# Performance work log

Hardware: AMD Instinct MI355X
Metric: run time of the kernel (lower is better)

Reference implementation:

```python
import jax, jax.numpy as jnp
import numpy as np

GRID = 16
N = GRID * GRID          # num_nodes = 256
D = 64                   # embed_dim
SPARSITY = 0.8
BATCH = 2048


def setup_inputs() -> dict:
    key = jax.random.key(0)
    ks = jax.random.split(key, 11)
    s1 = 1.0 / np.sqrt(D)          # fan_in of per-node Linears
    s2 = 1.0 / np.sqrt(N * D)      # fan_in of global_pool first Linear
    x = jax.random.normal(ks[0], (BATCH, N * D), dtype=jnp.float32)
    adj_param = jax.random.normal(ks[1], (N, N), dtype=jnp.float32) * 0.1
    W1 = jax.random.uniform(ks[2], (N, D, D), minval=-s1, maxval=s1, dtype=jnp.float32)
    b1 = jax.random.uniform(ks[3], (N, D), minval=-s1, maxval=s1, dtype=jnp.float32)
    W2 = jax.random.uniform(ks[4], (N, D, D), minval=-s1, maxval=s1, dtype=jnp.float32)
    b2 = jax.random.uniform(ks[5], (N, D), minval=-s1, maxval=s1, dtype=jnp.float32)
    gpW1 = jax.random.uniform(ks[6], (N * D, D), minval=-s2, maxval=s2, dtype=jnp.float32)
    gpb1 = jax.random.uniform(ks[7], (D,), minval=-s2, maxval=s2, dtype=jnp.float32)
    gpW2 = jax.random.uniform(ks[8], (D, D // 2), minval=-s1, maxval=s1, dtype=jnp.float32)
    gpb2 = jax.random.uniform(ks[9], (D // 2,), minval=-s1, maxval=s1, dtype=jnp.float32)
    return {"x": x, "adj_param": adj_param, "W1": W1, "b1": b1, "W2": W2, "b2": b2,
            "gpW1": gpW1, "gpb1": gpb1, "gpW2": gpW2, "gpb2": gpb2}


def _adjacency(adj_param):
    adj = jax.nn.sigmoid(adj_param)
    # threshold = sorted(flat adj)[int(sparsity * N*N)], then hard-threshold, then zero diagonal
    thr = jnp.sort(adj.reshape(-1))[int(SPARSITY * N * N)]
    adj = adj * (adj > thr)
    return adj * (1.0 - jnp.eye(N, dtype=adj.dtype))


def reference(x, adj_param, W1, b1, W2, b2, gpW1, gpb1, gpW2, gpb2):
    B = x.shape[0]
    adj = _adjacency(adj_param)
    xn = x.reshape(B, N, D)                                    # [B, N, D]
    # per-node distinct MLP == grouped GEMM with weights [N, D, D]
    h = jax.nn.relu(jnp.einsum('bnd,nde->bne', xn, W1) + b1)   # [B, N, D]
    node = jnp.einsum('bnd,nde->bne', h, W2) + b2              # [B, N, D]
    # adjacency-weighted neighbor sum: mixed[b,i] = sum_j adj[i,j] * node[b,j]
    mixed = jnp.einsum('ij,bjd->bid', adj, node)               # [B, N, D]
    final = 0.5 * mixed + 0.5 * node                           # residual mix
    g = jax.nn.relu(final.reshape(B, N * D) @ gpW1 + gpb1)     # [B, D]
    out = g @ gpW2 + gpb2                                      # [B, D//2]
    return out, adj
```

## Files before the change

### kernel.cpp

```cpp
#include <hip/hip_runtime.h>
#include <math.h>

typedef unsigned int uint;
typedef unsigned short ushort;
typedef short short8 __attribute__((ext_vector_type(8)));
typedef float f32x4 __attribute__((ext_vector_type(4)));

#define B_ 2048
#define N_ 256
#define D_ 64
#define ND_ 16384
#define NN_ 65536
#define KIDX_ 52428u
#define NGROUPS 32

#define WS_W1T    ((size_t)0)
#define WS_W2T    ((size_t)2*1024*1024)
#define WS_EFF    ((size_t)4*1024*1024)
#define WS_GPARTS ((size_t)8*1024*1024)
#define WS_SCAL   ((size_t)24*1024*1024)

__device__ __forceinline__ ushort f2bf(float f) {
    uint u = __float_as_uint(f);
    u += 0x7fffu + ((u >> 16) & 1u);
    return (ushort)(u >> 16);
}
__device__ __forceinline__ float bf2f(ushort u) { return __uint_as_float(((uint)u) << 16); }

__device__ __forceinline__ float sigmoid_exact(float a) {
    float t = (float)exp(-(double)a);
    return 1.0f / (1.0f + t);
}

__device__ __forceinline__ uint f2key(uint bits) {
    return bits ^ ((bits & 0x80000000u) ? 0xFFFFFFFFu : 0x80000000u);
}

__device__ __forceinline__ int wfrag_off(int e, int k) {
    return ((((e >> 4) * 2 + (k >> 5)) * 4 + ((k >> 3) & 3)) * 16 + (e & 15)) * 8 + (k & 7);
}

__device__ __forceinline__ int afrag_off(int jl, int i) {
    return (((((jl >> 4) * 8 + (i >> 5)) * 4 + ((i >> 3) & 3)) * 16) + (jl & 15)) * 8 + (i & 7);
}

__global__ __launch_bounds__(1024) void k_cvt_radix(const float* __restrict__ W1,
                                                    const float* __restrict__ W2,
                                                    const float* __restrict__ adj_param,
                                                    ushort* __restrict__ W1f,
                                                    ushort* __restrict__ W2f,
                                                    uint* __restrict__ scal) {
    __shared__ uint SH[16402] __attribute__((aligned(16)));
    int bid = blockIdx.x, tid = threadIdx.x;

    if (bid != 0) {
        int q = tid >> 8, t = tid & 255;
        int m = (bid - 1) * 4 + q;
        ushort* P = (ushort*)SH + q * 4096;
        const float* src = (m < 256) ? W1 + (size_t)m * 4096 : W2 + (size_t)(m - 256) * 4096;
#pragma unroll
        for (int i = 0; i < 16; i++) {
            int idx = i * 256 + t;
            int k = idx >> 6, e = idx & 63;
            P[wfrag_off(e, k)] = f2bf(src[idx]);
        }
        __syncthreads();
        ushort* dst = (m < 256) ? W1f + (size_t)m * 4096 : W2f + (size_t)(m - 256) * 4096;
#pragma unroll
        for (int i = 0; i < 2; i++)
            ((uint4*)dst)[i * 256 + t] = ((const uint4*)P)[i * 256 + t];
        return;
    }

    uint* hist = SH;
    uint* wsum = SH + 16384;
    uint* bc   = SH + 16400;
    const uint4* pv = (const uint4*)adj_param;
    uint rank = KIDX_;
    uint pref = 0u;
#pragma unroll 1
    for (int lvl = 0; lvl < 3; lvl++) {
        int nb  = (lvl == 2) ? 1024 : 2048;
        int sh  = (lvl == 0) ? 21 : (lvl == 1) ? 10 : 0;
        uint pm = (lvl == 0) ? 0u : (lvl == 1) ? 0xFFE00000u : 0xFFFFFC00u;
        for (int i = tid; i < nb * 8; i += 1024) hist[i] = 0u;
        __syncthreads();
        int sub = tid & 7;
#pragma unroll 1
        for (int i = 0; i < 16; i++) {
            uint4 v = pv[i * 1024 + tid];
#define H_(B) { uint k_ = f2key(B); if (((k_ ^ pref) & pm) == 0u) \
                atomicAdd(&hist[(((k_ >> sh) & (uint)(nb - 1)) << 3) + sub], 1u); }
            H_(v.x) H_(v.y) H_(v.z) H_(v.w)
#undef H_
        }
        __syncthreads();
        int bpt = nb >> 10;
        int b0 = tid * bpt;
        uint c0 = 0, c1 = 0;
#pragma unroll
        for (int k = 0; k < 8; k++) c0 += hist[(b0 << 3) + k];
        if (bpt == 2) {
#pragma unroll
            for (int k = 0; k < 8; k++) c1 += hist[((b0 + 1) << 3) + k];
        }
        uint s = c0 + c1;
        uint sc = s;
#pragma unroll
        for (int o = 1; o < 64; o <<= 1) {
            uint t2 = __shfl_up(sc, o, 64);
            if ((tid & 63) >= o) sc += t2;
        }
        if ((tid & 63) == 63) wsum[tid >> 6] = sc;
        __syncthreads();
        uint base = 0;
        for (int w = 0; w < (tid >> 6); w++) base += wsum[w];
        uint c = base + sc - s;
        if (rank >= c && rank < c + c0) { bc[0] = (uint)b0; bc[1] = rank - c; }
        c += c0;
        if (bpt == 2 && rank >= c && rank < c + c1) { bc[0] = (uint)(b0 + 1); bc[1] = rank - c; }
        __syncthreads();
        pref |= bc[0] << sh;
        rank = bc[1];
        __syncthreads();
    }
    if (tid == 0) {
        uint key = pref;
        uint bits = (key & 0x80000000u) ? (key ^ 0x80000000u) : ~key;
        scal[0] = __float_as_uint(sigmoid_exact(__uint_as_float(bits)));
    }
}

__global__ __launch_bounds__(256) void k_threff(const float* __restrict__ adj_param,
                                                const uint* __restrict__ scal,
                                                const float* __restrict__ gpW1,
                                                float* __restrict__ adj_out,
                                                ushort* __restrict__ effF) {
    __shared__ ushort adjS[16384] __attribute__((aligned(16)));
    __shared__ ushort Bf[16384] __attribute__((aligned(16)));
    int d = blockIdx.x, jt = blockIdx.y, tid = threadIdx.x;
    float thr = __uint_as_float(scal[0]);

    {
        int jl = tid & 63;
        int jglob = jt * 64 + jl;
        int wrow = tid >> 6;
#pragma unroll 1
        for (int i = 0; i < 16; i++) {
            float p[4];
#pragma unroll
            for (int u = 0; u < 4; u++)
                p[u] = adj_param[(size_t)((i * 4 + u) * 4 + wrow) * 256 + jglob];
#pragma unroll
            for (int u = 0; u < 4; u++) {
                int ir = (i * 4 + u) * 4 + wrow;
                float s = sigmoid_exact(p[u]);
                float v = (s > thr && ir != jglob) ? s : 0.0f;
                adjS[afrag_off(jl, ir)] = f2bf(v);
                if (d == 0) adj_out[(size_t)ir * 256 + jglob] = v;
            }
        }
    }
#pragma unroll
    for (int t = 0; t < 16; t++) {
        int idx = t * 256 + tid;
        int i = idx >> 4;
        int f4 = idx & 15;
        float4 v = *(const float4*)(gpW1 + ((size_t)i * 64 + d) * 64 + f4 * 4);
        int slab = i >> 6, il = i & 63, e0 = f4 * 4;
        Bf[slab * 4096 + wfrag_off(e0 + 0, il)] = f2bf(v.x);
        Bf[slab * 4096 + wfrag_off(e0 + 1, il)] = f2bf(v.y);
        Bf[slab * 4096 + wfrag_off(e0 + 2, il)] = f2bf(v.z);
        Bf[slab * 4096 + wfrag_off(e0 + 3, il)] = f2bf(v.w);
    }
    __syncthreads();
    int wid = tid >> 6, lane = tid & 63, quad = lane >> 4, l16 = lane & 15;
    f32x4 acc[4];
#pragma unroll
    for (int nt = 0; nt < 4; nt++) acc[nt] = (f32x4){0.f, 0.f, 0.f, 0.f};
#pragma unroll
    for (int ks8 = 0; ks8 < 8; ks8++) {
        short8 af = *(const short8*)&adjS[((((wid * 8 + ks8) * 4 + quad) * 16 + l16)) * 8];
        int slab = ks8 >> 1, ks = ks8 & 1;
#pragma unroll
        for (int nt = 0; nt < 4; nt++) {
            short8 bf = *(const short8*)&Bf[slab * 4096 + (((nt * 2 + ks) * 4 + quad) * 16 + l16) * 8];
            acc[nt] = __builtin_amdgcn_mfma_f32_16x16x32_bf16(af, bf, acc[nt], 0, 0, 0);
        }
    }
#pragma unroll
    for (int nt = 0; nt < 4; nt++) {
        int e = nt * 16 + l16;
#pragma unroll
        for (int r = 0; r < 4; r++) {
            int j = jt * 64 + wid * 16 + quad * 4 + r;
            float w = gpW1[((size_t)j * 64 + d) * 64 + e];
            float eff = 0.5f * (acc[nt][r] + w);
            effF[(size_t)j * 4096 + wfrag_off(e, d)] = f2bf(eff);
        }
    }
}

__global__ __launch_bounds__(256, 4) void k_fused(const float* __restrict__ x,
                                                  const ushort* __restrict__ W1f,
                                                  const ushort* __restrict__ W2f,
                                                  const ushort* __restrict__ effF,
                                                  const float* __restrict__ b1,
                                                  const float* __restrict__ b2,
                                                  float* __restrict__ gparts) {
    __shared__ ushort Wf1[4096] __attribute__((aligned(16)));
    __shared__ ushort Wf2[4096] __attribute__((aligned(16)));
    __shared__ ushort Ef[4096] __attribute__((aligned(16)));
    __shared__ ushort St[4][16 * 72];
    int tid = threadIdx.x;
    int g = blockIdx.x, bt = blockIdx.y;
    int wid = tid >> 6, lane = tid & 63, quad = lane >> 4, l16 = lane & 15;
    int rbase = bt * 64 + wid * 16;
    ushort* Sw = &St[wid][0];
    const float* xrow = x + (size_t)(rbase + l16) * ND_ + quad * 8;

    int n0 = g * 8;
    uint4 w1a = ((const uint4*)(W1f + (size_t)n0 * 4096))[tid];
    uint4 w1b = ((const uint4*)(W1f + (size_t)n0 * 4096))[256 + tid];
    uint4 w2a = ((const uint4*)(W2f + (size_t)n0 * 4096))[tid];
    uint4 w2b = ((const uint4*)(W2f + (size_t)n0 * 4096))[256 + tid];
    uint4 ea  = ((const uint4*)(effF + (size_t)n0 * 4096))[tid];
    uint4 eb  = ((const uint4*)(effF + (size_t)n0 * 4096))[256 + tid];
    float4 xr0, xr1, xr2, xr3;
    {
        const float* xp = xrow + (size_t)n0 * 64;
        xr0 = *(const float4*)(xp);
        xr1 = *(const float4*)(xp + 4);
        xr2 = *(const float4*)(xp + 32);
        xr3 = *(const float4*)(xp + 36);
    }
    float b1n[4], b2n[4];
#pragma unroll
    for (int nt = 0; nt < 4; nt++) {
        b1n[nt] = b1[n0 * 64 + nt * 16 + l16];
        b2n[nt] = b2[n0 * 64 + nt * 16 + l16];
    }
    ((uint4*)Wf1)[tid] = w1a;  ((uint4*)Wf1)[256 + tid] = w1b;
    ((uint4*)Wf2)[tid] = w2a;  ((uint4*)Wf2)[256 + tid] = w2b;
    ((uint4*)Ef)[tid]  = ea;   ((uint4*)Ef)[256 + tid]  = eb;

    f32x4 accg[4];
#pragma unroll
    for (int nt = 0; nt < 4; nt++) accg[nt] = (f32x4){0.f, 0.f, 0.f, 0.f};

    __syncthreads();

#pragma unroll 1
    for (int nl = 0; nl < 8; nl++) {
        short8 fa0, fa1;
        {
            short8 a;
            a[0] = (short)f2bf(xr0.x); a[1] = (short)f2bf(xr0.y);
            a[2] = (short)f2bf(xr0.z); a[3] = (short)f2bf(xr0.w);
            a[4] = (short)f2bf(xr1.x); a[5] = (short)f2bf(xr1.y);
            a[6] = (short)f2bf(xr1.z); a[7] = (short)f2bf(xr1.w);
            fa0 = a;
            short8 b;
            b[0] = (short)f2bf(xr2.x); b[1] = (short)f2bf(xr2.y);
            b[2] = (short)f2bf(xr2.z); b[3] = (short)f2bf(xr2.w);
            b[4] = (short)f2bf(xr3.x); b[5] = (short)f2bf(xr3.y);
            b[6] = (short)f2bf(xr3.z); b[7] = (short)f2bf(xr3.w);
            fa1 = b;
        }
        float bias1[4], bias2[4];
#pragma unroll
        for (int nt = 0; nt < 4; nt++) { bias1[nt] = b1n[nt]; bias2[nt] = b2n[nt]; }

        if (nl < 7) {
            int nn = g * 8 + nl + 1;
            w1a = ((const uint4*)(W1f + (size_t)nn * 4096))[tid];
            w1b = ((const uint4*)(W1f + (size_t)nn * 4096))[256 + tid];
            w2a = ((const uint4*)(W2f + (size_t)nn * 4096))[tid];
            w2b = ((const uint4*)(W2f + (size_t)nn * 4096))[256 + tid];
            ea  = ((const uint4*)(effF + (size_t)nn * 4096))[tid];
            eb  = ((const uint4*)(effF + (size_t)nn * 4096))[256 + tid];
            const float* xp = xrow + (size_t)nn * 64;
            xr0 = *(const float4*)(xp);
            xr1 = *(const float4*)(xp + 4);
            xr2 = *(const float4*)(xp + 32);
            xr3 = *(const float4*)(xp + 36);
#pragma unroll
            for (int nt = 0; nt < 4; nt++) {
                b1n[nt] = b1[nn * 64 + nt * 16 + l16];
                b2n[nt] = b2[nn * 64 + nt * 16 + l16];
            }
        }

        f32x4 acc[4];
#pragma unroll
        for (int nt = 0; nt < 4; nt++) acc[nt] = (f32x4){0.f, 0.f, 0.f, 0.f};
#pragma unroll
        for (int nt = 0; nt < 4; nt++) {
            short8 bf = *(const short8*)&Wf1[(((nt * 2 + 0) * 4 + quad) * 16 + l16) * 8];
            acc[nt] = __builtin_amdgcn_mfma_f32_16x16x32_bf16(fa0, bf, acc[nt], 0, 0, 0);
        }
#pragma unroll
        for (int nt = 0; nt < 4; nt++) {
            short8 bf = *(const short8*)&Wf1[(((nt * 2 + 1) * 4 + quad) * 16 + l16) * 8];
            acc[nt] = __builtin_amdgcn_mfma_f32_16x16x32_bf16(fa1, bf, acc[nt], 0, 0, 0);
        }
#pragma unroll
        for (int nt = 0; nt < 4; nt++)
#pragma unroll
            for (int r = 0; r < 4; r++) {
                float h = fmaxf(acc[nt][r] + bias1[nt], 0.0f);
                Sw[(quad * 4 + r) * 72 + nt * 16 + l16] = f2bf(h);
            }
        f32x4 acc2[4];
#pragma unroll
        for (int nt = 0; nt < 4; nt++) acc2[nt] = (f32x4){0.f, 0.f, 0.f, 0.f};
#pragma unroll
        for (int ks = 0; ks < 2; ks++) {
            short8 a2 = *(const short8*)&Sw[l16 * 72 + ks * 32 + quad * 8];
#pragma unroll
            for (int nt = 0; nt < 4; nt++) {
                short8 bf = *(const short8*)&Wf2[(((nt * 2 + ks) * 4 + quad) * 16 + l16) * 8];
                acc2[nt] = __builtin_amdgcn_mfma_f32_16x16x32_bf16(a2, bf, acc2[nt], 0, 0, 0);
            }
        }
#pragma unroll
        for (int nt = 0; nt < 4; nt++)
#pragma unroll
            for (int r = 0; r < 4; r++) {
                float v = acc2[nt][r] + bias2[nt];
                Sw[(quad * 4 + r) * 72 + nt * 16 + l16] = f2bf(v);
            }
#pragma unroll
        for (int ks = 0; ks < 2; ks++) {
            short8 a3 = *(const short8*)&Sw[l16 * 72 + ks * 32 + quad * 8];
#pragma unroll
            for (int nt = 0; nt < 4; nt++) {
                short8 bf = *(const short8*)&Ef[(((nt * 2 + ks) * 4 + quad) * 16 + l16) * 8];
                accg[nt] = __builtin_amdgcn_mfma_f32_16x16x32_bf16(a3, bf, accg[nt], 0, 0, 0);
            }
        }

        if (nl < 7) {
            __syncthreads();
            ((uint4*)Wf1)[tid] = w1a;  ((uint4*)Wf1)[256 + tid] = w1b;
            ((uint4*)Wf2)[tid] = w2a;  ((uint4*)Wf2)[256 + tid] = w2b;
            ((uint4*)Ef)[tid]  = ea;   ((uint4*)Ef)[256 + tid]  = eb;
            __syncthreads();
        }
    }

    float* gp = gparts + ((size_t)g * B_ + bt * 64) * 64;
#pragma unroll
    for (int nt = 0; nt < 4; nt++)
#pragma unroll
        for (int r = 0; r < 4; r++) {
            int b_loc = wid * 16 + quad * 4 + r;
            int e = nt * 16 + l16;
            gp[b_loc * 64 + e] = accg[nt][r];
        }
}

__global__ __launch_bounds__(256) void k_gp2(const float* __restrict__ gparts,
                                             const float* __restrict__ gpb1,
                                             const float* __restrict__ gpW2,
                                             const float* __restrict__ gpb2,
                                             float* __restrict__ out) {
    __shared__ float gs[4][64];
    int b0 = blockIdx.x * 4, tid = threadIdx.x;
    int r = tid >> 6, e = tid & 63;
    float s = gpb1[e];
#pragma unroll
    for (int p = 0; p < NGROUPS; p++)
        s += gparts[((size_t)p * B_ + b0 + r) * 64 + e];
    gs[r][e] = fmaxf(s, 0.0f);
    __syncthreads();
    if (tid < 128) {
        int rr = tid >> 5, o = tid & 31;
        float a = gpb2[o];
#pragma unroll 8
        for (int k2 = 0; k2 < 64; k2++) a += gs[rr][k2] * gpW2[k2 * 32 + o];
        out[(size_t)(b0 + rr) * 32 + o] = a;
    }
}

extern "C" void kernel_launch(void* const* d_in, const int* in_sizes, int n_in,
                              void* d_out, int out_size, void* d_ws, size_t ws_size,
                              hipStream_t stream) {
    const float* x = (const float*)d_in[0];
    const float* adj_param = (const float*)d_in[1];
    const float* W1 = (const float*)d_in[2];
    const float* b1 = (const float*)d_in[3];
    const float* W2 = (const float*)d_in[4];
    const float* b2 = (const float*)d_in[5];
    const float* gpW1 = (const float*)d_in[6];
    const float* gpb1 = (const float*)d_in[7];
    const float* gpW2 = (const float*)d_in[8];
    const float* gpb2 = (const float*)d_in[9];

    float* out = (float*)d_out;
    float* adj_out = (float*)d_out + NN_;

    char* ws = (char*)d_ws;
    ushort* W1f = (ushort*)(ws + WS_W1T);
    ushort* W2f = (ushort*)(ws + WS_W2T);
    ushort* effF = (ushort*)(ws + WS_EFF);
    float* gparts = (float*)(ws + WS_GPARTS);
    uint* scal = (uint*)(ws + WS_SCAL);

    k_cvt_radix<<<129, 1024, 0, stream>>>(W1, W2, adj_param, W1f, W2f, scal);
    k_threff<<<dim3(64, 4), 256, 0, stream>>>(adj_param, scal, gpW1, adj_out, effF);
    k_fused<<<dim3(NGROUPS, 32), 256, 0, stream>>>(x, W1f, W2f, effF, b1, b2, gparts);
    k_gp2<<<512, 256, 0, stream>>>(gparts, gpb1, gpW2, gpb2, out);
}
```

Baseline: 273.5 us.

## Double block to 512 threads covering 128 batch rows, stage biases in LDS

The fused grouped-MLP kernel now uses 512-thread blocks, with 8 waves each handling 16 batch rows (128 rows per block). The grid's batch dimension drops from 32 to 16. Each node's weight slabs are loaded to LDS once per 128 rows instead of once per 64, which halves global weight traffic and gives each thread a single uint4 per matrix. Biases for all 8 nodes are preloaded into shared memory up front instead of being prefetched per node from global memory. The trade-off is more LDS per block and fewer blocks, which may reduce occupancy and make the per-node syncthreads barriers span more waves.

```diff
diff --git a/kernel.cpp b/kernel.cpp
--- a/kernel.cpp
+++ b/kernel.cpp
@@ -201,7 +201,7 @@
     }
 }
 
-__global__ __launch_bounds__(256, 4) void k_fused(const float* __restrict__ x,
+__global__ __launch_bounds__(512, 4) void k_fused(const float* __restrict__ x,
                                                   const ushort* __restrict__ W1f,
                                                   const ushort* __restrict__ W2f,
                                                   const ushort* __restrict__ effF,
@@ -211,21 +211,22 @@
     __shared__ ushort Wf1[4096] __attribute__((aligned(16)));
     __shared__ ushort Wf2[4096] __attribute__((aligned(16)));
     __shared__ ushort Ef[4096] __attribute__((aligned(16)));
-    __shared__ ushort St[4][16 * 72];
+    __shared__ ushort St[8][16 * 72];
+    __shared__ float Bs[2][8][64];
     int tid = threadIdx.x;
     int g = blockIdx.x, bt = blockIdx.y;
     int wid = tid >> 6, lane = tid & 63, quad = lane >> 4, l16 = lane & 15;
-    int rbase = bt * 64 + wid * 16;
+    int rbase = bt * 128 + wid * 16;
     ushort* Sw = &St[wid][0];
     const float* xrow = x + (size_t)(rbase + l16) * ND_ + quad * 8;
 
+    ((float*)Bs[0])[tid] = b1[(size_t)g * 512 + tid];
+    ((float*)Bs[1])[tid] = b2[(size_t)g * 512 + tid];
+
     int n0 = g * 8;
     uint4 w1a = ((const uint4*)(W1f + (size_t)n0 * 4096))[tid];
-    uint4 w1b = ((const uint4*)(W1f + (size_t)n0 * 4096))[256 + tid];
     uint4 w2a = ((const uint4*)(W2f + (size_t)n0 * 4096))[tid];
-    uint4 w2b = ((const uint4*)(W2f + (size_t)n0 * 4096))[256 + tid];
     uint4 ea  = ((const uint4*)(effF + (size_t)n0 * 4096))[tid];
-    uint4 eb  = ((const uint4*)(effF + (size_t)n0 * 4096))[256 + tid];
     float4 xr0, xr1, xr2, xr3;
     {
         const float* xp = xrow + (size_t)n0 * 64;
@@ -234,15 +235,9 @@
         xr2 = *(const float4*)(xp + 32);
         xr3 = *(const float4*)(xp + 36);
     }
-    float b1n[4], b2n[4];
-#pragma unroll
-    for (int nt = 0; nt < 4; nt++) {
-        b1n[nt] = b1[n0 * 64 + nt * 16 + l16];
-        b2n[nt] = b2[n0 * 64 + nt * 16 + l16];
-    }
-    ((uint4*)Wf1)[tid] = w1a;  ((uint4*)Wf1)[256 + tid] = w1b;
-    ((uint4*)Wf2)[tid] = w2a;  ((uint4*)Wf2)[256 + tid] = w2b;
-    ((uint4*)Ef)[tid]  = ea;   ((uint4*)Ef)[256 + tid]  = eb;
+    ((uint4*)Wf1)[tid] = w1a;
+    ((uint4*)Wf2)[tid] = w2a;
+    ((uint4*)Ef)[tid]  = ea;
 
     f32x4 accg[4];
 #pragma unroll
@@ -267,28 +262,24 @@
             b[6] = (short)f2bf(xr3.z); b[7] = (short)f2bf(xr3.w);
             fa1 = b;
         }
-        float bias1[4], bias2[4];
-#pragma unroll
-        for (int nt = 0; nt < 4; nt++) { bias1[nt] = b1n[nt]; bias2[nt] = b2n[nt]; }
 
         if (nl < 7) {
             int nn = g * 8 + nl + 1;
             w1a = ((const uint4*)(W1f + (size_t)nn * 4096))[tid];
-            w1b = ((const uint4*)(W1f + (size_t)nn * 4096))[256 + tid];
             w2a = ((const uint4*)(W2f + (size_t)nn * 4096))[tid];
-            w2b = ((const uint4*)(W2f + (size_t)nn * 4096))[256 + tid];
             ea  = ((const uint4*)(effF + (size_t)nn * 4096))[tid];
-            eb  = ((const uint4*)(effF + (size_t)nn * 4096))[256 + tid];
             const float* xp = xrow + (size_t)nn * 64;
             xr0 = *(const float4*)(xp);
             xr1 = *(const float4*)(xp + 4);
             xr2 = *(const float4*)(xp + 32);
             xr3 = *(const float4*)(xp + 36);
-#pragma unroll
-            for (int nt = 0; nt < 4; nt++) {
-                b1n[nt] = b1[nn * 64 + nt * 16 + l16];
-                b2n[nt] = b2[nn * 64 + nt * 16 + l16];
-            }
+        }
+
+        float bias1[4], bias2[4];
+#pragma unroll
+        for (int nt = 0; nt < 4; nt++) {
+            bias1[nt] = Bs[0][nl][nt * 16 + l16];
+            bias2[nt] = Bs[1][nl][nt * 16 + l16];
         }
 
         f32x4 acc[4];
@@ -342,14 +333,14 @@
 
         if (nl < 7) {
             __syncthreads();
-            ((uint4*)Wf1)[tid] = w1a;  ((uint4*)Wf1)[256 + tid] = w1b;
-            ((uint4*)Wf2)[tid] = w2a;  ((uint4*)Wf2)[256 + tid] = w2b;
-            ((uint4*)Ef)[tid]  = ea;   ((uint4*)Ef)[256 + tid]  = eb;
+            ((uint4*)Wf1)[tid] = w1a;
+            ((uint4*)Wf2)[tid] = w2a;
+            ((uint4*)Ef)[tid]  = ea;
             __syncthreads();
         }
     }
 
-    float* gp = gparts + ((size_t)g * B_ + bt * 64) * 64;
+    float* gp = gparts + ((size_t)g * B_ + bt * 128) * 64;
 #pragma unroll
     for (int nt = 0; nt < 4; nt++)
 #pragma unroll
@@ -409,6 +400,6 @@
 
     k_cvt_radix<<<129, 1024, 0, stream>>>(W1, W2, adj_param, W1f, W2f, scal);
     k_threff<<<dim3(64, 4), 256, 0, stream>>>(adj_param, scal, gpW1, adj_out, effF);
-    k_fused<<<dim3(NGROUPS, 32), 256, 0, stream>>>(x, W1f, W2f, effF, b1, b2, gparts);
+    k_fused<<<dim3(NGROUPS, 16), 512, 0, stream>>>(x, W1f, W2f, effF, b1, b2, gparts);
     k_gp2<<<512, 256, 0, stream>>>(gparts, gpb1, gpW2, gpb2, out);
 }
```

Result: no change. 270.2 us (median of 2 runs) (-1.2%).
